# Optimization experiments

Hardware: AMD Instinct MI355X
Metric: run time of the kernel (lower is better)

## Reference

```python
import jax, jax.numpy as jnp
import numpy as np

B, L, D, H, DFF, V, NL = 8, 512, 1024, 16, 4096, 32000, 6
DH = D // H
EPS = 1e-5


def _layer_norm(x):
    # fresh nn.LayerNorm(d_model) each call: gamma=1, beta=0
    mu = jnp.mean(x, axis=-1, keepdims=True)
    var = jnp.var(x, axis=-1, keepdims=True)
    return (x - mu) / jnp.sqrt(var + EPS)


def _positional_encoding(seq_len, d_model, dtype):
    position = jnp.arange(seq_len, dtype=jnp.float32)[:, None]
    div_term = 1.0 / jnp.power(10000.0, jnp.arange(0, d_model, 2, dtype=jnp.float32) / d_model)
    pe = jnp.zeros((seq_len, d_model), dtype=jnp.float32)
    pe = pe.at[:, 0::2].set(jnp.sin(position * div_term))
    pe = pe.at[:, 1::2].set(jnp.cos(position * div_term))
    return pe.astype(dtype)  # [L, D]


def setup_inputs() -> dict:
    key = jax.random.key(0)
    ks = jax.random.split(key, 16)
    s = 0.02
    inp = {
        "sequence": jax.random.randint(ks[0], (B, L), 0, V),
        "segment_label": jax.random.randint(ks[1], (B, L), 0, 3),
        "tok_emb": jax.random.normal(ks[2], (V, D), jnp.float32) * s,
        "seg_emb": jax.random.normal(ks[3], (3, D), jnp.float32) * s,
        "Wq": jax.random.normal(ks[4], (NL, D, D), jnp.float32) * s,
        "bq": jnp.zeros((NL, D), jnp.float32),
        "Wk": jax.random.normal(ks[5], (NL, D, D), jnp.float32) * s,
        "bk": jnp.zeros((NL, D), jnp.float32),
        "Wv": jax.random.normal(ks[6], (NL, D, D), jnp.float32) * s,
        "bv": jnp.zeros((NL, D), jnp.float32),
        "Wo": jax.random.normal(ks[7], (NL, D, D), jnp.float32) * s,
        "bo": jnp.zeros((NL, D), jnp.float32),
        "W1": jax.random.normal(ks[8], (NL, D, DFF), jnp.float32) * s,
        "b1": jnp.zeros((NL, DFF), jnp.float32),
        "W2": jax.random.normal(ks[9], (NL, DFF, D), jnp.float32) * s,
        "b2": jnp.zeros((NL, D), jnp.float32),
    }
    return inp


def reference(sequence, segment_label, tok_emb, seg_emb, Wq, bq, Wk, bk, Wv, bv, Wo, bo, W1, b1, W2, b2):
    n_layers = Wq.shape[0]
    batch, seq_len = sequence.shape
    d_model = tok_emb.shape[1]
    n_heads = H
    dh = d_model // n_heads

    # pad mask: True where key token == 0; broadcast over heads and query positions
    pad = (sequence == 0)  # [B, Lk]
    mask = pad[:, None, None, :]  # [B, 1, 1, Lk]

    pe = _positional_encoding(seq_len, d_model, tok_emb.dtype)
    x = tok_emb[sequence] + pe[None, :, :] + seg_emb[segment_label]  # [B, L, D]

    for i in range(n_layers):
        residual = x
        # NOTE: original code uses a raw reshape [B, L, H*dh] -> [B, H, L, dh]
        # (no transpose); we replicate that exact math.
        q = (x @ Wq[i] + bq[i]).reshape(batch, n_heads, seq_len, dh)
        k = (x @ Wk[i] + bk[i]).reshape(batch, n_heads, seq_len, dh)
        v = (x @ Wv[i] + bv[i]).reshape(batch, n_heads, seq_len, dh)
        scores = jnp.einsum("bhqd,bhkd->bhqk", q, k) / jnp.sqrt(jnp.asarray(dh, x.dtype))
        scores = jnp.where(mask, jnp.asarray(-1e9, x.dtype), scores)
        attn = jax.nn.softmax(scores, axis=-1)
        context = jnp.einsum("bhqk,bhkd->bhqd", attn, v).reshape(batch, seq_len, n_heads * dh)
        out = context @ Wo[i] + bo[i]
        x = _layer_norm(out + residual)

        residual = x
        h = jax.nn.gelu(x @ W1[i] + b1[i], approximate=False)
        out = h @ W2[i] + b2[i]
        x = _layer_norm(residual + out)

    return x
```

## Files before the change

### kernel.cpp

```cpp
#include <hip/hip_runtime.h>
#include <cstdint>
#include <cstddef>

typedef unsigned short u16;
typedef __attribute__((ext_vector_type(8))) short short8;
typedef __attribute__((ext_vector_type(4))) float f32x4;

#define DEV __device__ __forceinline__

DEV float bf2f(u16 u) {
    union { float f; uint32_t i; } c; c.i = ((uint32_t)u) << 16; return c.f;
}
DEV u16 f2bf(float f) {
    union { float f; uint32_t i; } c; c.f = f;
    uint32_t r = c.i + 0x7FFF + ((c.i >> 16) & 1);
    return (u16)(r >> 16);
}

DEV void gload16(const void* g, void* l) {
    __builtin_amdgcn_global_load_lds(
        (const __attribute__((address_space(1))) void*)g,
        (__attribute__((address_space(3))) void*)l, 16, 0, 0);
}

template<int WM, int WN, int MR, int NR, int EPI>
__global__ __launch_bounds__(256)
void gemm_bt(const u16* __restrict__ A, const u16* __restrict__ B, void* __restrict__ C,
             const float* __restrict__ bias, const float* __restrict__ resid,
             int K, int lda, int ldb, int ldc,
             int nh, long a_zb, long a_zh, long b_zb, long b_zh, long c_zb, long c_zh,
             float scale)
{
    static_assert(WM * WN == 4, "4 waves");
    constexpr int BM = WM * MR * 16;
    constexpr int BN = WN * NR * 16;
    constexpr int BK = 32;
    __shared__ __align__(16) u16 As[2 * BM * BK];
    __shared__ __align__(16) u16 Bs[2 * BN * BK];

    const int tid  = threadIdx.x;
    const int lane = tid & 63;
    const int wid  = tid >> 6;
    const int zz = blockIdx.z;
    const int b = zz / nh, h = zz % nh;
    A += (long)b * a_zb + (long)h * a_zh;
    B += (long)b * b_zb + (long)h * b_zh;
    const long coff = (long)b * c_zb + (long)h * c_zh;
    const int m0 = blockIdx.x * BM, n0 = blockIdx.y * BN;

    f32x4 acc[MR][NR] = {};
    constexpr int AI = (BM * 4) / 256;
    constexpr int BI = (BN * 4) / 256;

    const int wr = wid / WN, wc = wid % WN;
    const int lr = lane & 15, lk = lane >> 4;

    auto stage = [&](int buf, int k0) {
#pragma unroll
        for (int i = 0; i < AI; ++i) {
            int ch = (i << 8) + tid;
            const u16* g = A + (long)(m0 + (ch >> 2)) * lda + k0 + ((ch & 3) << 3);
            gload16(g, (char*)As + (size_t)buf * (BM * BK * 2) + ch * 16);
        }
#pragma unroll
        for (int i = 0; i < BI; ++i) {
            int ch = (i << 8) + tid;
            const u16* g = B + (long)(n0 + (ch >> 2)) * ldb + k0 + ((ch & 3) << 3);
            gload16(g, (char*)Bs + (size_t)buf * (BN * BK * 2) + ch * 16);
        }
    };

    stage(0, 0);
    asm volatile("s_waitcnt vmcnt(0)" ::: "memory");
    __syncthreads();

    int cur = 0;
    for (int k0 = 0; k0 < K; k0 += BK) {
        if (k0 + BK < K) stage(cur ^ 1, k0 + BK);

        const u16* Ac = As + (size_t)cur * (BM * BK);
        const u16* Bc = Bs + (size_t)cur * (BN * BK);
        short8 af[MR], bf[NR];
#pragma unroll
        for (int m = 0; m < MR; ++m)
            af[m] = *(const short8*)(Ac + (wr * MR * 16 + m * 16 + lr) * BK + lk * 8);
#pragma unroll
        for (int n = 0; n < NR; ++n)
            bf[n] = *(const short8*)(Bc + (wc * NR * 16 + n * 16 + lr) * BK + lk * 8);
#pragma unroll
        for (int m = 0; m < MR; ++m)
#pragma unroll
            for (int n = 0; n < NR; ++n)
                acc[m][n] = __builtin_amdgcn_mfma_f32_16x16x32_bf16(af[m], bf[n], acc[m][n], 0, 0, 0);

        asm volatile("s_waitcnt vmcnt(0)" ::: "memory");
        __syncthreads();
        cur ^= 1;
    }

#pragma unroll
    for (int m = 0; m < MR; ++m) {
        const int rowb = m0 + wr * MR * 16 + m * 16 + (lane >> 4) * 4;
#pragma unroll
        for (int n = 0; n < NR; ++n) {
            const int col = n0 + wc * NR * 16 + n * 16 + lr;
            float bv = 0.f;
            if (EPI == 0 || EPI == 1 || EPI == 2 || EPI == 5) bv = bias[col];
#pragma unroll
            for (int j = 0; j < 4; ++j) {
                const long idx = coff + (long)(rowb + j) * ldc + col;
                float v = acc[m][n][j];
                if (EPI == 0) {
                    ((u16*)C)[idx] = f2bf(v + bv);
                } else if (EPI == 1) {
                    ((float*)C)[idx] = v + bv + resid[(long)(rowb + j) * ldc + col];
                } else if (EPI == 2) {
                    float t = v + bv;
                    ((u16*)C)[idx] = f2bf(0.5f * t * (1.0f + erff(t * 0.70710678118654752f)));
                } else if (EPI == 3) {
                    ((u16*)C)[idx] = f2bf(v * scale);
                } else if (EPI == 5) {
                    const long qidx = (long)(col >> 10) * 4194304L
                                    + (long)(rowb + j) * 1024 + (col & 1023);
                    ((u16*)C)[qidx] = f2bf(v + bv);
                } else {
                    ((u16*)C)[idx] = f2bf(v);
                }
            }
        }
    }
}

__global__ __launch_bounds__(256)
void wconv_kernel(const float* __restrict__ src, u16* __restrict__ dst,
                  int K, int N, int row_off)
{
    __shared__ __align__(16) float t[64][65];
    const float* s = src + (long)(blockIdx.y * 64) * N + blockIdx.x * 64;
    const int tid = threadIdx.x;
#pragma unroll
    for (int i = 0; i < 4; ++i) {
        int ch = (i << 8) + tid;
        int r = ch >> 4, c4 = ch & 15;
        float4 v = *(const float4*)(s + (long)r * N + c4 * 4);
        t[r][c4 * 4 + 0] = v.x; t[r][c4 * 4 + 1] = v.y;
        t[r][c4 * 4 + 2] = v.z; t[r][c4 * 4 + 3] = v.w;
    }
    __syncthreads();
    u16* d = dst + (long)(row_off + blockIdx.x * 64) * K + blockIdx.y * 64;
#pragma unroll
    for (int i = 0; i < 4; ++i) {
        int ch = (i << 8) + tid;
        int c = ch >> 4, k4 = ch & 15;
        ushort4 o;
        o.x = f2bf(t[k4 * 4 + 0][c]);
        o.y = f2bf(t[k4 * 4 + 1][c]);
        o.z = f2bf(t[k4 * 4 + 2][c]);
        o.w = f2bf(t[k4 * 4 + 3][c]);
        *(ushort4*)(d + (long)c * K + k4 * 4) = o;
    }
}

__global__ __launch_bounds__(256)
void bconcat_kernel(const float* __restrict__ bq, const float* __restrict__ bk,
                    const float* __restrict__ bv, float* __restrict__ out)
{
    int i = blockIdx.x * 256 + threadIdx.x;
    int l = i / 3072, n = i % 3072;
    float v = (n < 1024) ? bq[l * 1024 + n]
            : (n < 2048) ? bk[l * 1024 + n - 1024]
                         : bv[l * 1024 + n - 2048];
    out[i] = v;
}

__global__ __launch_bounds__(256)
void embed_kernel(const int* __restrict__ seq, const int* __restrict__ seg,
                  const float* __restrict__ tok, const float* __restrict__ sege,
                  float* __restrict__ x, u16* __restrict__ xb)
{
    long i = ((long)blockIdx.x << 8) + threadIdx.x;
    int d2 = (int)(i & 511);
    long bl = i >> 9;
    int l = (int)(bl & 511);
    int t = seq[bl];
    int g = seg[bl];
    float div = powf(10000.f, -(float)(2 * d2) * (1.0f / 1024.f));
    float arg = (float)l * div;
    float sv = sinf(arg), cv = cosf(arg);
    long toff = (long)t * 1024 + 2 * d2;
    long goff = (long)g * 1024 + 2 * d2;
    float x0 = tok[toff]     + sv + sege[goff];
    float x1 = tok[toff + 1] + cv + sege[goff + 1];
    long xo = (bl << 10) + 2 * d2;
    x[xo] = x0; x[xo + 1] = x1;
    xb[xo] = f2bf(x0); xb[xo + 1] = f2bf(x1);
}

__global__ __launch_bounds__(256)
void vtrans_kernel(const u16* __restrict__ Vb, u16* __restrict__ vt)
{
    __shared__ __align__(16) u16 t[64][72];
    const int bh = blockIdx.y;
    const int l0 = blockIdx.x << 6;
    const u16* src = Vb + ((long)bh << 15) + (long)l0 * 64;
    const int tid = threadIdx.x;
#pragma unroll
    for (int i = 0; i < 2; ++i) {
        int ch = (i << 8) + tid;
        int r = ch >> 3, c8 = ch & 7;
        short8 v = *(const short8*)(src + (long)r * 64 + (c8 << 3));
#pragma unroll
        for (int j = 0; j < 8; ++j) t[r][(c8 << 3) + j] = (u16)v[j];
    }
    __syncthreads();
    u16* d = vt + ((long)bh << 15) + l0;
#pragma unroll
    for (int i = 0; i < 2; ++i) {
        int ch = (i << 8) + tid;
        int dd = ch >> 3, l8 = ch & 7;
        short8 o;
#pragma unroll
        for (int j = 0; j < 8; ++j) o[j] = (short)t[(l8 << 3) + j][dd];
        *(short8*)(d + (long)dd * 512 + (l8 << 3)) = o;
    }
}

__global__ __launch_bounds__(256)
void softmax_kernel(u16* __restrict__ S, const int* __restrict__ seq)
{
    long row = ((long)blockIdx.x << 2) + (threadIdx.x >> 6);
    int lane = threadIdx.x & 63;
    int b = (int)(row >> 13);
    u16* p = S + (row << 9);
    short8 raw = *(short8*)(p + (lane << 3));
    const int* sq = seq + (b << 9) + (lane << 3);
    float v[8];
#pragma unroll
    for (int i = 0; i < 8; ++i)
        v[i] = (sq[i] == 0) ? -1e9f : bf2f((u16)raw[i]);
    float mx = v[0];
#pragma unroll
    for (int i = 1; i < 8; ++i) mx = fmaxf(mx, v[i]);
#pragma unroll
    for (int o = 32; o; o >>= 1) mx = fmaxf(mx, __shfl_xor(mx, o));
    float e[8], sum = 0.f;
#pragma unroll
    for (int i = 0; i < 8; ++i) { e[i] = expf(v[i] - mx); sum += e[i]; }
#pragma unroll
    for (int o = 32; o; o >>= 1) sum += __shfl_xor(sum, o);
    float r = 1.0f / sum;
    short8 o8;
#pragma unroll
    for (int i = 0; i < 8; ++i) o8[i] = (short)f2bf(e[i] * r);
    *(short8*)(p + (lane << 3)) = o8;
}

__global__ __launch_bounds__(256)
void ln_kernel(const float* __restrict__ in, float* __restrict__ xout, u16* __restrict__ xbout)
{
    const int row = blockIdx.x;
    const int tid = threadIdx.x;
    const float4 v = ((const float4*)(in + (long)row * 1024))[tid];
    float s = v.x + v.y + v.z + v.w;
#pragma unroll
    for (int o = 32; o; o >>= 1) s += __shfl_down(s, o);
    __shared__ float red[8];
    const int wid = tid >> 6, lane = tid & 63;
    if (lane == 0) red[wid] = s;
    __syncthreads();
    const float mean = (red[0] + red[1] + red[2] + red[3]) * (1.0f / 1024.f);
    const float dx = v.x - mean, dy = v.y - mean, dz = v.z - mean, dw = v.w - mean;
    float q = dx * dx + dy * dy + dz * dz + dw * dw;
#pragma unroll
    for (int o = 32; o; o >>= 1) q += __shfl_down(q, o);
    if (lane == 0) red[4 + wid] = q;
    __syncthreads();
    const float var = (red[4] + red[5] + red[6] + red[7]) * (1.0f / 1024.f);
    const float inv = rsqrtf(var + 1e-5f);
    float4 o4;
    o4.x = dx * inv; o4.y = dy * inv; o4.z = dz * inv; o4.w = dw * inv;
    ((float4*)(xout + (long)row * 1024))[tid] = o4;
    ushort4 ob;
    ob.x = f2bf(o4.x); ob.y = f2bf(o4.y); ob.z = f2bf(o4.z); ob.w = f2bf(o4.w);
    ((ushort4*)(xbout + (long)row * 1024))[tid] = ob;
}

extern "C" void kernel_launch(void* const* d_in, const int* in_sizes, int n_in,
                              void* d_out, int out_size, void* d_ws, size_t ws_size,
                              hipStream_t stream)
{
    const int*   seqp = (const int*)d_in[0];
    const int*   segp = (const int*)d_in[1];
    const float* tok  = (const float*)d_in[2];
    const float* sege = (const float*)d_in[3];
    const float* Wq = (const float*)d_in[4];  const float* bq = (const float*)d_in[5];
    const float* Wk = (const float*)d_in[6];  const float* bk = (const float*)d_in[7];
    const float* Wv = (const float*)d_in[8];  const float* bv = (const float*)d_in[9];
    const float* Wo = (const float*)d_in[10]; const float* bo = (const float*)d_in[11];
    const float* W1 = (const float*)d_in[12]; const float* b1 = (const float*)d_in[13];
    const float* W2 = (const float*)d_in[14]; const float* b2 = (const float*)d_in[15];

    char* w = (char*)d_ws;
    auto take = [&](size_t bytes) -> void* {
        void* p = (void*)w; w += (bytes + 255) & ~(size_t)255; return p;
    };
    float* x    = (float*)take(4096UL * 1024 * 4);
    u16*   xb   = (u16*)  take(4096UL * 1024 * 2);
    float* tmp  = (float*)take(4096UL * 1024 * 4);
    u16*   R1   = (u16*)  take(128UL * 512 * 512 * 2);
    u16*   qkv3 = (u16*)  take(3UL * 4096 * 1024 * 2);
    u16*   ctx  = (u16*)  take(4096UL * 1024 * 2);
    u16*   vt   = (u16*)  take(128UL * 64 * 512 * 2);
    u16*   qkvw = (u16*)  take(3072UL * 1024 * 2);
    u16*   wo_t = (u16*)  take(1024UL * 1024 * 2);
    u16*   w1_t = (u16*)  take(4096UL * 1024 * 2);
    u16*   w2_t = (u16*)  take(1024UL * 4096 * 2);
    float* bqkv = (float*)take(6UL * 3072 * 4);

    u16* S    = R1;
    u16* hbuf = R1;
    u16* Qb   = qkv3;
    u16* Kb   = qkv3 + 4194304L;
    u16* Vb   = qkv3 + 8388608L;

    bconcat_kernel<<<72, 256, 0, stream>>>(bq, bk, bv, bqkv);
    embed_kernel<<<8192, 256, 0, stream>>>(seqp, segp, tok, sege, x, xb);

    for (int l = 0; l < 6; ++l) {
        wconv_kernel<<<dim3(16, 16), 256, 0, stream>>>(Wq + (long)l * 1048576L, qkvw, 1024, 1024, 0);
        wconv_kernel<<<dim3(16, 16), 256, 0, stream>>>(Wk + (long)l * 1048576L, qkvw, 1024, 1024, 1024);
        wconv_kernel<<<dim3(16, 16), 256, 0, stream>>>(Wv + (long)l * 1048576L, qkvw, 1024, 1024, 2048);
        wconv_kernel<<<dim3(16, 16), 256, 0, stream>>>(Wo + (long)l * 1048576L, wo_t, 1024, 1024, 0);
        wconv_kernel<<<dim3(64, 16), 256, 0, stream>>>(W1 + (long)l * 4194304L, w1_t, 1024, 4096, 0);
        wconv_kernel<<<dim3(16, 64), 256, 0, stream>>>(W2 + (long)l * 4194304L, w2_t, 4096, 1024, 0);

        gemm_bt<2, 2, 4, 4, 5><<<dim3(32, 24, 1), 256, 0, stream>>>(
            xb, qkvw, qkv3, bqkv + l * 3072, nullptr,
            1024, 1024, 1024, 1024, 1, 0, 0, 0, 0, 0, 0, 1.f);

        vtrans_kernel<<<dim3(8, 128), 256, 0, stream>>>(Vb, vt);

        gemm_bt<2, 2, 4, 4, 3><<<dim3(4, 4, 128), 256, 0, stream>>>(
            Qb, Kb, S, nullptr, nullptr,
            64, 64, 64, 512,
            16, 524288L, 32768L, 524288L, 32768L, 4194304L, 262144L, 0.125f);

        softmax_kernel<<<16384, 256, 0, stream>>>(S, seqp);

        gemm_bt<4, 1, 2, 4, 4><<<dim3(4, 1, 128), 256, 0, stream>>>(
            S, vt, ctx, nullptr, nullptr,
            512, 512, 512, 64,
            16, 4194304L, 262144L, 524288L, 32768L, 524288L, 32768L, 1.f);

        gemm_bt<2, 2, 4, 4, 1><<<dim3(32, 8, 1), 256, 0, stream>>>(
            ctx, wo_t, tmp, bo + l * 1024, x,
            1024, 1024, 1024, 1024, 1, 0, 0, 0, 0, 0, 0, 1.f);

        ln_kernel<<<4096, 256, 0, stream>>>(tmp, x, xb);

        gemm_bt<2, 2, 4, 4, 2><<<dim3(32, 32, 1), 256, 0, stream>>>(
            xb, w1_t, hbuf, b1 + l * 4096, nullptr,
            1024, 1024, 1024, 4096, 1, 0, 0, 0, 0, 0, 0, 1.f);

        gemm_bt<2, 2, 4, 4, 1><<<dim3(32, 8, 1), 256, 0, stream>>>(
            hbuf, w2_t, tmp, b2 + l * 1024, x,
            4096, 4096, 4096, 1024, 1, 0, 0, 0, 0, 0, 0, 1.f);

        ln_kernel<<<4096, 256, 0, stream>>>(tmp, (l == 5) ? (float*)d_out : x, xb);
    }
}
```

Baseline: 1.949 ms.

## Triple-buffer GEMM LDS staging with partial vmcnt waits

Moves the bf16 GEMM main loop from double to triple buffering in LDS. Tiles are prefetched three K-steps ahead and waits use partial vmcnt counts, so later loads can stay in flight while the current tile is computed. Fragments are read into registers and the block syncs on a barrier before the freed buffer is refilled, so that refill overlaps the MFMA work. The cost is 50% more LDS per block, which may lower occupancy. Wait counts not in the helper's table fall back to vmcnt(0), which is safe but loses the overlap.

```diff
diff --git a/kernel.cpp b/kernel.cpp
--- a/kernel.cpp
+++ b/kernel.cpp
@@ -21,6 +21,15 @@
     __builtin_amdgcn_global_load_lds(
         (const __attribute__((address_space(1))) void*)g,
         (__attribute__((address_space(3))) void*)l, 16, 0, 0);
+}
+
+template<int N> DEV void waitv() {
+    if constexpr (N == 0)      asm volatile("s_waitcnt vmcnt(0)" ::: "memory");
+    else if constexpr (N == 3) asm volatile("s_waitcnt vmcnt(3)" ::: "memory");
+    else if constexpr (N == 4) asm volatile("s_waitcnt vmcnt(4)" ::: "memory");
+    else if constexpr (N == 6) asm volatile("s_waitcnt vmcnt(6)" ::: "memory");
+    else if constexpr (N == 8) asm volatile("s_waitcnt vmcnt(8)" ::: "memory");
+    else                       asm volatile("s_waitcnt vmcnt(0)" ::: "memory");
 }
 
 template<int WM, int WN, int MR, int NR, int EPI>
@@ -35,8 +44,9 @@
     constexpr int BM = WM * MR * 16;
     constexpr int BN = WN * NR * 16;
     constexpr int BK = 32;
-    __shared__ __align__(16) u16 As[2 * BM * BK];
-    __shared__ __align__(16) u16 Bs[2 * BN * BK];
+    constexpr int NBUF = 3;
+    __shared__ __align__(16) u16 As[NBUF * BM * BK];
+    __shared__ __align__(16) u16 Bs[NBUF * BN * BK];
 
     const int tid  = threadIdx.x;
     const int lane = tid & 63;
@@ -51,6 +61,7 @@
     f32x4 acc[MR][NR] = {};
     constexpr int AI = (BM * 4) / 256;
     constexpr int BI = (BN * 4) / 256;
+    constexpr int L  = AI + BI;
 
     const int wr = wid / WN, wc = wid % WN;
     const int lr = lane & 15, lk = lane >> 4;
@@ -70,14 +81,18 @@
         }
     };
 
-    stage(0, 0);
-    asm volatile("s_waitcnt vmcnt(0)" ::: "memory");
-    __syncthreads();
-
-    int cur = 0;
-    for (int k0 = 0; k0 < K; k0 += BK) {
-        if (k0 + BK < K) stage(cur ^ 1, k0 + BK);
-
+    const int nt = K >> 5;
+
+    if (nt > 0) stage(0, 0);
+    if (nt > 1) stage(1, BK);
+    if (nt > 2) stage(2, 2 * BK);
+    if (nt > 2)      waitv<2 * L>();
+    else if (nt > 1) waitv<L>();
+    else             waitv<0>();
+    __builtin_amdgcn_s_barrier();
+
+    for (int k = 0; k < nt; ++k) {
+        const int cur = k % 3;
         const u16* Ac = As + (size_t)cur * (BM * BK);
         const u16* Bc = Bs + (size_t)cur * (BN * BK);
         short8 af[MR], bf[NR];
@@ -87,15 +102,24 @@
 #pragma unroll
         for (int n = 0; n < NR; ++n)
             bf[n] = *(const short8*)(Bc + (wc * NR * 16 + n * 16 + lr) * BK + lk * 8);
+
+        asm volatile("s_waitcnt lgkmcnt(0)" ::: "memory");
+        __builtin_amdgcn_s_barrier();
+
+        if (k + 3 < nt) stage(cur, (k + 3) * BK);
+
 #pragma unroll
         for (int m = 0; m < MR; ++m)
 #pragma unroll
             for (int n = 0; n < NR; ++n)
                 acc[m][n] = __builtin_amdgcn_mfma_f32_16x16x32_bf16(af[m], bf[n], acc[m][n], 0, 0, 0);
 
-        asm volatile("s_waitcnt vmcnt(0)" ::: "memory");
-        __syncthreads();
-        cur ^= 1;
+        if (k + 1 < nt) {
+            if (k + 4 <= nt)      waitv<2 * L>();
+            else if (k + 3 == nt) waitv<L>();
+            else                  waitv<0>();
+            __builtin_amdgcn_s_barrier();
+        }
     }
 
 #pragma unroll
```

Result: faster. 1.861 ms (-4.5%).
